# Kernel optimization log

Hardware: AMD Instinct MI355X
Metric: run time of the kernel (lower is better)

## Reference

```python
import jax, jax.numpy as jnp
import numpy as np

E = 16          # num_local_experts
K = 4           # experts_per_token
H = 2048        # hidden_size
I = 2048        # intermediate_size
LIMIT = 7.0     # swiglu_limit
ALPHA = 1.702   # glu_alpha


def setup_inputs() -> dict:
    key = jax.random.key(0)
    ks = jax.random.split(key, 9)
    int8 = lambda k, shp: jax.random.randint(k, shp, -127, 128).astype(jnp.float32)
    return {
        "hidden_states": jax.random.normal(ks[0], (1024, H), dtype=jnp.float32),
        "router_logits": jax.random.normal(ks[1], (1024, E), dtype=jnp.float32),
        "gate_up_proj": int8(ks[2], (E, H, 2 * I)),                      # int8 values in f32
        "gate_up_proj_scale": jax.random.uniform(ks[3], (E, 2 * I), minval=0.5, maxval=1.5) * 0.002,
        "gate_up_proj_bias": jax.random.normal(ks[4], (E, 2 * I), dtype=jnp.float32) * 0.01,
        "gate_up_smooth_scale": jnp.ones((E, I), dtype=jnp.float32),
        "down_proj": int8(ks[5], (E, I, H)),
        "down_proj_scale": jax.random.uniform(ks[6], (E, H), minval=0.5, maxval=1.5) * 0.002,
        "down_proj_bias": jax.random.normal(ks[7], (E, H), dtype=jnp.float32) * 0.01,
    }


def _dyn_quant(x):
    # per-token symmetric int8 dynamic quant (npu_dynamic_quant)
    scale = jnp.maximum(jnp.max(jnp.abs(x), axis=-1, keepdims=True) / 127.0, 1e-8)
    q = jnp.clip(jnp.round(x / scale), -127.0, 127.0)
    return q, scale


def reference(hidden_states, router_logits, gate_up_proj, gate_up_proj_scale,
              gate_up_proj_bias, gate_up_smooth_scale, down_proj,
              down_proj_scale, down_proj_bias):
    T = hidden_states.shape[0]
    C = (2 * T * K) // E

    # --- gating (npu_moe_gating_top_k: softmax + top-k, then renormalize) ---
    probs = jax.nn.softmax(router_logits, axis=-1)
    topk_w, topk_i = jax.lax.top_k(probs, K)                 # [T,K]
    topk_w = topk_w / jnp.sum(topk_w, axis=-1, keepdims=True)

    # --- per-token dynamic quant ---
    x_q, x_scale = _dyn_quant(hidden_states)                 # [T,H], [T,1]

    # --- dispatch (npu_moe_init_routing_v2): token-major expansion, capacity buckets ---
    flat_e = topk_i.reshape(-1)                              # [T*K] expert id per row
    flat_w = topk_w.reshape(-1)                              # [T*K]
    src = jnp.arange(T * K) // K                             # [T*K] source token
    onehot = jax.nn.one_hot(flat_e, E, dtype=jnp.int32)      # [T*K,E]
    pos = jnp.sum(jnp.cumsum(onehot, axis=0) * onehot, axis=1) - 1  # position within expert
    valid = pos < C
    slot = flat_e * C + jnp.where(valid, pos, 0)             # unique for valid rows
    vf = valid.astype(x_q.dtype)[:, None]
    x_disp = jnp.zeros((E * C, H), x_q.dtype).at[slot].add(x_q[src] * vf)
    s_disp = jnp.zeros((E * C, 1), x_scale.dtype).at[slot].add(x_scale[src] * vf)
    x_disp = x_disp.reshape(E, C, H)
    s_disp = s_disp.reshape(E, C, 1)

    gu_i32 = jnp.einsum('ech,ehf->ecf', x_disp, gate_up_proj)          # [E,C,2I]
    y = gu_i32 * s_disp * gate_up_proj_scale[:, None, :] + gate_up_proj_bias[:, None, :]

    # --- gpt-oss swiglu (activate_left, clamp_limit, alpha=1.702, glu_bias=1.0) ---
    gate = jnp.minimum(y[..., :I], LIMIT)
    up = jnp.clip(y[..., I:], -LIMIT, LIMIT)
    act = gate * jax.nn.sigmoid(ALPHA * gate) * (up + 1.0)
    act = act * gate_up_smooth_scale[:, None, :]

    # --- requant + grouped GEMM 2 + dequant ---
    h_q, h_scale = _dyn_quant(act)                                     # [E,C,I], [E,C,1]
    z_i32 = jnp.einsum('eci,eih->ech', h_q, down_proj)                 # [E,C,H]
    z = z_i32 * h_scale * down_proj_scale[:, None, :] + down_proj_bias[:, None, :]

    # --- combine (npu_moe_finalize_routing): weighted scatter-add per source token ---
    gathered = z.reshape(E * C, H)[slot]                               # [T*K,H]
    out = jnp.zeros((T, H), z.dtype).at[src].add(flat_w[:, None] * vf * gathered)
    return out
```

## Files before the change

### kernel.cpp

```cpp
#include <hip/hip_runtime.h>
#include <stdint.h>
#include <stddef.h>

#define T_TOK 1024
#define NE    16
#define TOPK  4
#define HID   2048
#define INTER 2048
#define CAP   512
#define GLIMIT 7.0f
#define GALPHA 1.702f

#define BM  128
#define BK  32
#define LDP 40

typedef __attribute__((ext_vector_type(8))) _Float16 half8;
typedef __attribute__((ext_vector_type(4))) float     f32x4;

__global__ __launch_bounds__(256) void gating_kernel(
    const float* __restrict__ logits, int* __restrict__ topki, float* __restrict__ topkw)
{
    int t = blockIdx.x * 256 + threadIdx.x;
    if (t >= T_TOK) return;
    float l[NE];
#pragma unroll
    for (int e = 0; e < NE; e++) l[e] = logits[t * NE + e];
    unsigned used = 0;
    float val[TOPK]; int idx[TOPK];
#pragma unroll
    for (int k = 0; k < TOPK; k++) {
        float bv = -3.4e38f; int bi = 0;
#pragma unroll
        for (int e = 0; e < NE; e++) {
            bool ok = (((used >> e) & 1u) == 0u) && (l[e] > bv);
            bv = ok ? l[e] : bv;
            bi = ok ? e : bi;
        }
        used |= (1u << bi); idx[k] = bi; val[k] = bv;
    }
    float m = val[0];
    float s = 0.f, w[TOPK];
#pragma unroll
    for (int k = 0; k < TOPK; k++) { w[k] = expf(val[k] - m); s += w[k]; }
    float inv = 1.0f / s;
#pragma unroll
    for (int k = 0; k < TOPK; k++) { topki[t * TOPK + k] = idx[k]; topkw[t * TOPK + k] = w[k] * inv; }
}

__global__ __launch_bounds__(256) void quant_x_kernel(
    const float* __restrict__ x, _Float16* __restrict__ xq, float* __restrict__ xs)
{
    int t = blockIdx.x;
    const float* row = x + (size_t)t * HID;
    __shared__ float red[256];
    float amax = 0.f;
    for (int i = threadIdx.x; i < HID; i += 256) amax = fmaxf(amax, fabsf(row[i]));
    red[threadIdx.x] = amax; __syncthreads();
    for (int s = 128; s > 0; s >>= 1) {
        if (threadIdx.x < s) red[threadIdx.x] = fmaxf(red[threadIdx.x], red[threadIdx.x + s]);
        __syncthreads();
    }
    float scale = fmaxf(red[0] / 127.0f, 1e-8f);
    if (threadIdx.x == 0) xs[t] = scale;
    for (int i = threadIdx.x; i < HID; i += 256) {
        float q = rintf(row[i] / scale);
        q = fminf(fmaxf(q, -127.f), 127.f);
        xq[(size_t)t * HID + i] = (_Float16)q;
    }
}

__global__ __launch_bounds__(1024) void routing_kernel(
    const int* __restrict__ topki, const float* __restrict__ topkw,
    int* __restrict__ row_src, float* __restrict__ row_w, int* __restrict__ counts)
{
    int wv = threadIdx.x >> 6;
    int lane = threadIdx.x & 63;
    int base = 0;
    for (int r0 = 0; r0 < T_TOK * TOPK; r0 += 64) {
        int r = r0 + lane;
        int e = topki[r];
        unsigned long long mask = __ballot(e == wv);
        int pre = __popcll(mask & ((1ULL << lane) - 1ULL));
        if (e == wv) {
            int pos = base + pre;
            if (pos < CAP) {
                row_src[wv * CAP + pos] = r >> 2;
                row_w[wv * CAP + pos] = topkw[r];
            }
        }
        base += __popcll(mask);
    }
    if (lane == 0) counts[wv] = (base < CAP) ? base : CAP;
}

__global__ __launch_bounds__(256) void gemm1_kernel(
    const _Float16* __restrict__ xq, const float* __restrict__ xs,
    const int* __restrict__ row_src, const int* __restrict__ counts,
    const float* __restrict__ gup, const float* __restrict__ gus,
    const float* __restrict__ gub, const float* __restrict__ smo,
    float* __restrict__ act)
{
    int nt = blockIdx.x;
    int mt = blockIdx.y;
    int e  = blockIdx.z;
    int count = counts[e];
    int m0 = mt * BM;
    if (m0 >= count) return;

    __shared__ _Float16 sA[BM * LDP];
    __shared__ _Float16 sB[128 * LDP];

    int t = threadIdx.x;
    int lane = t & 63, w = t >> 6;
    int n16 = lane & 15, quad = lane >> 4;

    int aM = t >> 1, aHalf = t & 1;
    int agr = m0 + aM;
    const _Float16* aptr = nullptr;
    if (agr < count) aptr = xq + (size_t)row_src[e * CAP + agr] * HID;

    f32x4 acc[2][8];
#pragma unroll
    for (int i = 0; i < 2; i++)
#pragma unroll
        for (int j = 0; j < 8; j++) acc[i][j] = (f32x4)0.0f;

    const float* gbase = gup + (size_t)e * HID * (2 * INTER);

    for (int k0 = 0; k0 < HID; k0 += BK) {
        __syncthreads();
        {
            int4 v0, v1;
            v0.x = v0.y = v0.z = v0.w = 0; v1 = v0;
            if (aptr) {
                const int4* s4 = (const int4*)(aptr + k0 + aHalf * 16);
                v0 = s4[0]; v1 = s4[1];
            }
            int4* d4 = (int4*)&sA[aM * LDP + aHalf * 16];
            d4[0] = v0; d4[1] = v1;
        }
        {
            int n = t & 63;
            int kr = (t >> 6) * 8;
#pragma unroll
            for (int h = 0; h < 2; h++) {
                const float* src = gbase + (size_t)(k0 + kr) * (2 * INTER) + h * INTER + nt * 64 + n;
#pragma unroll
                for (int i = 0; i < 8; i++)
                    sB[(h * 64 + n) * LDP + kr + i] = (_Float16)src[(size_t)i * (2 * INTER)];
            }
        }
        __syncthreads();

        half8 af[2], bfr[8];
#pragma unroll
        for (int mf = 0; mf < 2; mf++)
            af[mf] = *(const half8*)&sA[(w * 32 + mf * 16 + n16) * LDP + quad * 8];
#pragma unroll
        for (int nf = 0; nf < 8; nf++)
            bfr[nf] = *(const half8*)&sB[(nf * 16 + n16) * LDP + quad * 8];
#pragma unroll
        for (int mf = 0; mf < 2; mf++)
#pragma unroll
            for (int nf = 0; nf < 8; nf++)
                acc[mf][nf] = __builtin_amdgcn_mfma_f32_16x16x32_f16(af[mf], bfr[nf], acc[mf][nf], 0, 0, 0);
    }

    const float* gsc = gus + (size_t)e * (2 * INTER);
    const float* gbi = gub + (size_t)e * (2 * INTER);
    const float* sms = smo + (size_t)e * INTER;
#pragma unroll
    for (int mf = 0; mf < 2; mf++) {
#pragma unroll
        for (int r = 0; r < 4; r++) {
            int gr = m0 + w * 32 + mf * 16 + quad * 4 + r;
            if (gr >= count) continue;
            float srow = xs[row_src[e * CAP + gr]];
            float* arow = act + (size_t)(e * CAP + gr) * INTER;
#pragma unroll
            for (int g = 0; g < 4; g++) {
                int col = nt * 64 + g * 16 + n16;
                float yg = acc[mf][g][r]     * srow * gsc[col]         + gbi[col];
                float yu = acc[mf][g + 4][r] * srow * gsc[INTER + col] + gbi[INTER + col];
                float gate = fminf(yg, GLIMIT);
                float up   = fminf(fmaxf(yu, -GLIMIT), GLIMIT);
                float sig  = 1.0f / (1.0f + expf(-GALPHA * gate));
                arow[col] = gate * sig * (up + 1.0f) * sms[col];
            }
        }
    }
}

__global__ __launch_bounds__(256) void requant_kernel(
    const float* __restrict__ act, const int* __restrict__ counts,
    _Float16* __restrict__ hq, float* __restrict__ hs)
{
    int b = blockIdx.x;
    int e = b >> 9, c = b & (CAP - 1);
    if (c >= counts[e]) return;
    const float* row = act + (size_t)b * INTER;
    __shared__ float red[256];
    float amax = 0.f;
    for (int i = threadIdx.x; i < INTER; i += 256) amax = fmaxf(amax, fabsf(row[i]));
    red[threadIdx.x] = amax; __syncthreads();
    for (int s = 128; s > 0; s >>= 1) {
        if (threadIdx.x < s) red[threadIdx.x] = fmaxf(red[threadIdx.x], red[threadIdx.x + s]);
        __syncthreads();
    }
    float scale = fmaxf(red[0] / 127.0f, 1e-8f);
    if (threadIdx.x == 0) hs[b] = scale;
    for (int i = threadIdx.x; i < INTER; i += 256) {
        float q = rintf(row[i] / scale);
        q = fminf(fmaxf(q, -127.f), 127.f);
        hq[(size_t)b * INTER + i] = (_Float16)q;
    }
}

__global__ __launch_bounds__(256) void gemm2_kernel(
    const _Float16* __restrict__ hq, const float* __restrict__ hs,
    const int* __restrict__ row_src, const float* __restrict__ row_w,
    const int* __restrict__ counts, const float* __restrict__ dwn,
    const float* __restrict__ dsc, const float* __restrict__ dbi,
    float* __restrict__ out)
{
    int nt = blockIdx.x;
    int mt = blockIdx.y;
    int e  = blockIdx.z;
    int count = counts[e];
    int m0 = mt * BM;
    if (m0 >= count) return;

    __shared__ _Float16 sA[BM * LDP];
    __shared__ _Float16 sB[128 * LDP];

    int t = threadIdx.x;
    int lane = t & 63, w = t >> 6;
    int n16 = lane & 15, quad = lane >> 4;

    int aM = t >> 1, aHalf = t & 1;
    int agr = m0 + aM;
    const _Float16* aptr = nullptr;
    if (agr < count) aptr = hq + (size_t)(e * CAP + agr) * INTER;

    f32x4 acc[2][8];
#pragma unroll
    for (int i = 0; i < 2; i++)
#pragma unroll
        for (int j = 0; j < 8; j++) acc[i][j] = (f32x4)0.0f;

    const float* bbase = dwn + (size_t)e * INTER * HID;

    for (int k0 = 0; k0 < INTER; k0 += BK) {
        __syncthreads();
        {
            int4 v0, v1;
            v0.x = v0.y = v0.z = v0.w = 0; v1 = v0;
            if (aptr) {
                const int4* s4 = (const int4*)(aptr + k0 + aHalf * 16);
                v0 = s4[0]; v1 = s4[1];
            }
            int4* d4 = (int4*)&sA[aM * LDP + aHalf * 16];
            d4[0] = v0; d4[1] = v1;
        }
        {
            int n = t & 127;
            int kr = (t >> 7) * 16;
            const float* src = bbase + (size_t)(k0 + kr) * HID + nt * 128 + n;
#pragma unroll
            for (int i = 0; i < 16; i++)
                sB[n * LDP + kr + i] = (_Float16)src[(size_t)i * HID];
        }
        __syncthreads();

        half8 af[2], bfr[8];
#pragma unroll
        for (int mf = 0; mf < 2; mf++)
            af[mf] = *(const half8*)&sA[(w * 32 + mf * 16 + n16) * LDP + quad * 8];
#pragma unroll
        for (int nf = 0; nf < 8; nf++)
            bfr[nf] = *(const half8*)&sB[(nf * 16 + n16) * LDP + quad * 8];
#pragma unroll
        for (int mf = 0; mf < 2; mf++)
#pragma unroll
            for (int nf = 0; nf < 8; nf++)
                acc[mf][nf] = __builtin_amdgcn_mfma_f32_16x16x32_f16(af[mf], bfr[nf], acc[mf][nf], 0, 0, 0);
    }

    const float* dscE = dsc + (size_t)e * HID;
    const float* dbiE = dbi + (size_t)e * HID;
#pragma unroll
    for (int mf = 0; mf < 2; mf++) {
#pragma unroll
        for (int r = 0; r < 4; r++) {
            int gr = m0 + w * 32 + mf * 16 + quad * 4 + r;
            if (gr >= count) continue;
            int ri = e * CAP + gr;
            float hsr = hs[ri];
            float wr  = row_w[ri];
            float* orow = out + (size_t)row_src[ri] * HID;
#pragma unroll
            for (int nf = 0; nf < 8; nf++) {
                int col = nt * 128 + nf * 16 + n16;
                float z = acc[mf][nf][r] * hsr * dscE[col] + dbiE[col];
                atomicAdd(&orow[col], wr * z);
            }
        }
    }
}

extern "C" void kernel_launch(void* const* d_in, const int* in_sizes, int n_in,
                              void* d_out, int out_size, void* d_ws, size_t ws_size,
                              hipStream_t stream)
{
    (void)in_sizes; (void)n_in; (void)out_size; (void)ws_size;
    const float* x   = (const float*)d_in[0];
    const float* rl  = (const float*)d_in[1];
    const float* gup = (const float*)d_in[2];
    const float* gus = (const float*)d_in[3];
    const float* gub = (const float*)d_in[4];
    const float* smo = (const float*)d_in[5];
    const float* dwn = (const float*)d_in[6];
    const float* dsc = (const float*)d_in[7];
    const float* dbi = (const float*)d_in[8];
    float* out = (float*)d_out;

    char* p = (char*)d_ws;
    auto carve = [&](size_t bytes) -> char* {
        char* r = p; p += (bytes + 255) & ~(size_t)255; return r;
    };
    _Float16* xq   = (_Float16*)carve((size_t)T_TOK * HID * 2);
    float* xs      = (float*)carve((size_t)T_TOK * 4);
    int* topki     = (int*)carve((size_t)T_TOK * TOPK * 4);
    float* topkw   = (float*)carve((size_t)T_TOK * TOPK * 4);
    int* counts    = (int*)carve((size_t)NE * 4);
    int* rsrc      = (int*)carve((size_t)NE * CAP * 4);
    float* rw      = (float*)carve((size_t)NE * CAP * 4);
    float* actb    = (float*)carve((size_t)NE * CAP * INTER * 4);
    _Float16* hq   = (_Float16*)carve((size_t)NE * CAP * INTER * 2);
    float* hsb     = (float*)carve((size_t)NE * CAP * 4);

    hipMemsetAsync(d_out, 0, (size_t)T_TOK * HID * 4, stream);
    gating_kernel<<<dim3((T_TOK + 255) / 256), 256, 0, stream>>>(rl, topki, topkw);
    quant_x_kernel<<<dim3(T_TOK), 256, 0, stream>>>(x, xq, xs);
    routing_kernel<<<dim3(1), 1024, 0, stream>>>(topki, topkw, rsrc, rw, counts);
    gemm1_kernel<<<dim3(INTER / 64, CAP / BM, NE), 256, 0, stream>>>(
        xq, xs, rsrc, counts, gup, gus, gub, smo, actb);
    requant_kernel<<<dim3(NE * CAP), 256, 0, stream>>>(actb, counts, hq, hsb);
    gemm2_kernel<<<dim3(HID / 128, CAP / BM, NE), 256, 0, stream>>>(
        hq, hsb, rsrc, rw, counts, dwn, dsc, dbi, out);
}
```

Measured before the change: 1.081 ms.

## Switch grouped GEMMs to int8 MFMA with pre-packed int8 weight tiles

Result: no change. 1.094 ms (+1.2%).

```diff
diff --git a/kernel.cpp b/kernel.cpp
--- a/kernel.cpp
+++ b/kernel.cpp
@@ -12,11 +12,16 @@
 #define GALPHA 1.702f
 
 #define BM  128
-#define BK  32
-#define LDP 40
-
-typedef __attribute__((ext_vector_type(8))) _Float16 half8;
-typedef __attribute__((ext_vector_type(4))) float     f32x4;
+#define BK  64
+
+typedef __attribute__((ext_vector_type(4))) int   iv4;
+typedef __attribute__((ext_vector_type(4))) float f32x4;
+
+typedef const __attribute__((address_space(1))) unsigned gl_u32;
+typedef __attribute__((address_space(3))) unsigned lds_u32;
+__device__ __forceinline__ void gl_lds16(const void* g, void* l) {
+    __builtin_amdgcn_global_load_lds((gl_u32*)g, (lds_u32*)l, 16, 0, 0);
+}
 
 __global__ __launch_bounds__(256) void gating_kernel(
     const float* __restrict__ logits, int* __restrict__ topki, float* __restrict__ topkw)
@@ -49,13 +54,16 @@
 }
 
 __global__ __launch_bounds__(256) void quant_x_kernel(
-    const float* __restrict__ x, _Float16* __restrict__ xq, float* __restrict__ xs)
+    const float* __restrict__ x, char* __restrict__ xq, float* __restrict__ xs)
 {
     int t = blockIdx.x;
-    const float* row = x + (size_t)t * HID;
+    const float4* row = (const float4*)(x + (size_t)t * HID);
     __shared__ float red[256];
     float amax = 0.f;
-    for (int i = threadIdx.x; i < HID; i += 256) amax = fmaxf(amax, fabsf(row[i]));
+    float4 v0 = row[threadIdx.x];
+    float4 v1 = row[threadIdx.x + 256];
+    amax = fmaxf(amax, fmaxf(fmaxf(fabsf(v0.x), fabsf(v0.y)), fmaxf(fabsf(v0.z), fabsf(v0.w))));
+    amax = fmaxf(amax, fmaxf(fmaxf(fabsf(v1.x), fabsf(v1.y)), fmaxf(fabsf(v1.z), fabsf(v1.w))));
     red[threadIdx.x] = amax; __syncthreads();
     for (int s = 128; s > 0; s >>= 1) {
         if (threadIdx.x < s) red[threadIdx.x] = fmaxf(red[threadIdx.x], red[threadIdx.x + s]);
@@ -63,10 +71,19 @@
     }
     float scale = fmaxf(red[0] / 127.0f, 1e-8f);
     if (threadIdx.x == 0) xs[t] = scale;
-    for (int i = threadIdx.x; i < HID; i += 256) {
-        float q = rintf(row[i] / scale);
-        q = fminf(fmaxf(q, -127.f), 127.f);
-        xq[(size_t)t * HID + i] = (_Float16)q;
+    char4* orow = (char4*)(xq + (size_t)t * HID);
+    {
+        char4 c;
+        c.x = (char)fminf(fmaxf(rintf(v0.x / scale), -127.f), 127.f);
+        c.y = (char)fminf(fmaxf(rintf(v0.y / scale), -127.f), 127.f);
+        c.z = (char)fminf(fmaxf(rintf(v0.z / scale), -127.f), 127.f);
+        c.w = (char)fminf(fmaxf(rintf(v0.w / scale), -127.f), 127.f);
+        orow[threadIdx.x] = c;
+        c.x = (char)fminf(fmaxf(rintf(v1.x / scale), -127.f), 127.f);
+        c.y = (char)fminf(fmaxf(rintf(v1.y / scale), -127.f), 127.f);
+        c.z = (char)fminf(fmaxf(rintf(v1.z / scale), -127.f), 127.f);
+        c.w = (char)fminf(fmaxf(rintf(v1.w / scale), -127.f), 127.f);
+        orow[threadIdx.x + 256] = c;
     }
 }
 
@@ -94,10 +111,36 @@
     if (lane == 0) counts[wv] = (base < CAP) ? base : CAP;
 }
 
+__global__ __launch_bounds__(128) void convw_kernel(
+    const float* __restrict__ src, char* __restrict__ dst, int pitch, int mode)
+{
+    int nt = blockIdx.x, kt = blockIdx.y, e = blockIdx.z;
+    int l = threadIdx.x;
+    int col;
+    if (mode == 0) col = (l < 64) ? (nt * 64 + l) : (INTER + nt * 64 + (l - 64));
+    else           col = nt * 128 + l;
+    const float* s = src + (size_t)e * 2048 * pitch + (size_t)(kt * 64) * pitch + col;
+    int wv[16];
+#pragma unroll
+    for (int j = 0; j < 16; j++) {
+        int v = 0;
+#pragma unroll
+        for (int bq = 0; bq < 4; bq++) {
+            int q = (int)s[(size_t)(j * 4 + bq) * pitch];
+            v |= (q & 0xff) << (8 * bq);
+        }
+        wv[j] = v;
+    }
+    int4* d = (int4*)(dst + (((size_t)e * gridDim.x + nt) * 32 + kt) * 8192 + l * 64);
+#pragma unroll
+    for (int j = 0; j < 4; j++)
+        d[j] = make_int4(wv[4 * j], wv[4 * j + 1], wv[4 * j + 2], wv[4 * j + 3]);
+}
+
 __global__ __launch_bounds__(256) void gemm1_kernel(
-    const _Float16* __restrict__ xq, const float* __restrict__ xs,
+    const char* __restrict__ xq, const float* __restrict__ xs,
     const int* __restrict__ row_src, const int* __restrict__ counts,
-    const float* __restrict__ gup, const float* __restrict__ gus,
+    const char* __restrict__ gpack, const float* __restrict__ gus,
     const float* __restrict__ gub, const float* __restrict__ smo,
     float* __restrict__ act)
 {
@@ -108,63 +151,52 @@
     int m0 = mt * BM;
     if (m0 >= count) return;
 
-    __shared__ _Float16 sA[BM * LDP];
-    __shared__ _Float16 sB[128 * LDP];
+    __shared__ char sA[BM * BK];
+    __shared__ char sB[128 * BK];
 
     int t = threadIdx.x;
     int lane = t & 63, w = t >> 6;
     int n16 = lane & 15, quad = lane >> 4;
 
-    int aM = t >> 1, aHalf = t & 1;
-    int agr = m0 + aM;
-    const _Float16* aptr = nullptr;
-    if (agr < count) aptr = xq + (size_t)row_src[e * CAP + agr] * HID;
-
-    f32x4 acc[2][8];
+    const char* aSrc[2];
+#pragma unroll
+    for (int op = 0; op < 2; op++) {
+        int c = op * 256 + t;
+        int row = c >> 2, ks = c & 3;
+        int gr = m0 + row;
+        if (gr > count - 1) gr = count - 1;
+        aSrc[op] = xq + (size_t)row_src[e * CAP + gr] * HID + ks * 16;
+    }
+    const char* bSrc = gpack + (((size_t)e * 32 + nt) * 32) * 8192 + t * 16;
+
+    iv4 acc[2][8];
 #pragma unroll
     for (int i = 0; i < 2; i++)
 #pragma unroll
-        for (int j = 0; j < 8; j++) acc[i][j] = (f32x4)0.0f;
-
-    const float* gbase = gup + (size_t)e * HID * (2 * INTER);
-
-    for (int k0 = 0; k0 < HID; k0 += BK) {
-        __syncthreads();
-        {
-            int4 v0, v1;
-            v0.x = v0.y = v0.z = v0.w = 0; v1 = v0;
-            if (aptr) {
-                const int4* s4 = (const int4*)(aptr + k0 + aHalf * 16);
-                v0 = s4[0]; v1 = s4[1];
-            }
-            int4* d4 = (int4*)&sA[aM * LDP + aHalf * 16];
-            d4[0] = v0; d4[1] = v1;
-        }
-        {
-            int n = t & 63;
-            int kr = (t >> 6) * 8;
-#pragma unroll
-            for (int h = 0; h < 2; h++) {
-                const float* src = gbase + (size_t)(k0 + kr) * (2 * INTER) + h * INTER + nt * 64 + n;
-#pragma unroll
-                for (int i = 0; i < 8; i++)
-                    sB[(h * 64 + n) * LDP + kr + i] = (_Float16)src[(size_t)i * (2 * INTER)];
-            }
-        }
-        __syncthreads();
-
-        half8 af[2], bfr[8];
+        for (int j = 0; j < 8; j++) acc[i][j] = (iv4)0;
+
+    for (int kt = 0; kt < HID / BK; kt++) {
+        __syncthreads();
+#pragma unroll
+        for (int op = 0; op < 2; op++)
+            gl_lds16(aSrc[op] + kt * BK, sA + op * 4096 + w * 1024);
+#pragma unroll
+        for (int op = 0; op < 2; op++)
+            gl_lds16(bSrc + kt * 8192 + op * 4096, sB + op * 4096 + w * 1024);
+        __syncthreads();
+
+        iv4 af[2], bf[8];
 #pragma unroll
         for (int mf = 0; mf < 2; mf++)
-            af[mf] = *(const half8*)&sA[(w * 32 + mf * 16 + n16) * LDP + quad * 8];
+            af[mf] = *(const iv4*)(sA + (w * 32 + mf * 16 + n16) * 64 + quad * 16);
 #pragma unroll
         for (int nf = 0; nf < 8; nf++)
-            bfr[nf] = *(const half8*)&sB[(nf * 16 + n16) * LDP + quad * 8];
+            bf[nf] = *(const iv4*)(sB + (nf * 16 + n16) * 64 + quad * 16);
 #pragma unroll
         for (int mf = 0; mf < 2; mf++)
 #pragma unroll
             for (int nf = 0; nf < 8; nf++)
-                acc[mf][nf] = __builtin_amdgcn_mfma_f32_16x16x32_f16(af[mf], bfr[nf], acc[mf][nf], 0, 0, 0);
+                acc[mf][nf] = __builtin_amdgcn_mfma_i32_16x16x64_i8(af[mf], bf[nf], acc[mf][nf], 0, 0, 0);
     }
 
     const float* gsc = gus + (size_t)e * (2 * INTER);
@@ -181,8 +213,8 @@
 #pragma unroll
             for (int g = 0; g < 4; g++) {
                 int col = nt * 64 + g * 16 + n16;
-                float yg = acc[mf][g][r]     * srow * gsc[col]         + gbi[col];
-                float yu = acc[mf][g + 4][r] * srow * gsc[INTER + col] + gbi[INTER + col];
+                float yg = (float)acc[mf][g][r]     * srow * gsc[col]         + gbi[col];
+                float yu = (float)acc[mf][g + 4][r] * srow * gsc[INTER + col] + gbi[INTER + col];
                 float gate = fminf(yg, GLIMIT);
                 float up   = fminf(fmaxf(yu, -GLIMIT), GLIMIT);
                 float sig  = 1.0f / (1.0f + expf(-GALPHA * gate));
@@ -194,15 +226,17 @@
 
 __global__ __launch_bounds__(256) void requant_kernel(
     const float* __restrict__ act, const int* __restrict__ counts,
-    _Float16* __restrict__ hq, float* __restrict__ hs)
+    char* __restrict__ hq, float* __restrict__ hs)
 {
     int b = blockIdx.x;
     int e = b >> 9, c = b & (CAP - 1);
     if (c >= counts[e]) return;
-    const float* row = act + (size_t)b * INTER;
+    const float4* row = (const float4*)(act + (size_t)b * INTER);
     __shared__ float red[256];
-    float amax = 0.f;
-    for (int i = threadIdx.x; i < INTER; i += 256) amax = fmaxf(amax, fabsf(row[i]));
+    float4 v0 = row[threadIdx.x];
+    float4 v1 = row[threadIdx.x + 256];
+    float amax = fmaxf(fmaxf(fabsf(v0.x), fabsf(v0.y)), fmaxf(fabsf(v0.z), fabsf(v0.w)));
+    amax = fmaxf(amax, fmaxf(fmaxf(fabsf(v1.x), fabsf(v1.y)), fmaxf(fabsf(v1.z), fabsf(v1.w))));
     red[threadIdx.x] = amax; __syncthreads();
     for (int s = 128; s > 0; s >>= 1) {
         if (threadIdx.x < s) red[threadIdx.x] = fmaxf(red[threadIdx.x], red[threadIdx.x + s]);
@@ -210,17 +244,26 @@
     }
     float scale = fmaxf(red[0] / 127.0f, 1e-8f);
     if (threadIdx.x == 0) hs[b] = scale;
-    for (int i = threadIdx.x; i < INTER; i += 256) {
-        float q = rintf(row[i] / scale);
-        q = fminf(fmaxf(q, -127.f), 127.f);
-        hq[(size_t)b * INTER + i] = (_Float16)q;
+    char4* orow = (char4*)(hq + (size_t)b * INTER);
+    {
+        char4 cc;
+        cc.x = (char)fminf(fmaxf(rintf(v0.x / scale), -127.f), 127.f);
+        cc.y = (char)fminf(fmaxf(rintf(v0.y / scale), -127.f), 127.f);
+        cc.z = (char)fminf(fmaxf(rintf(v0.z / scale), -127.f), 127.f);
+        cc.w = (char)fminf(fmaxf(rintf(v0.w / scale), -127.f), 127.f);
+        orow[threadIdx.x] = cc;
+        cc.x = (char)fminf(fmaxf(rintf(v1.x / scale), -127.f), 127.f);
+        cc.y = (char)fminf(fmaxf(rintf(v1.y / scale), -127.f), 127.f);
+        cc.z = (char)fminf(fmaxf(rintf(v1.z / scale), -127.f), 127.f);
+        cc.w = (char)fminf(fmaxf(rintf(v1.w / scale), -127.f), 127.f);
+        orow[threadIdx.x + 256] = cc;
     }
 }
 
 __global__ __launch_bounds__(256) void gemm2_kernel(
-    const _Float16* __restrict__ hq, const float* __restrict__ hs,
+    const char* __restrict__ hq, const float* __restrict__ hs,
     const int* __restrict__ row_src, const float* __restrict__ row_w,
-    const int* __restrict__ counts, const float* __restrict__ dwn,
+    const int* __restrict__ counts, const char* __restrict__ dpack,
     const float* __restrict__ dsc, const float* __restrict__ dbi,
     float* __restrict__ out)
 {
@@ -231,60 +274,52 @@
     int m0 = mt * BM;
     if (m0 >= count) return;
 
-    __shared__ _Float16 sA[BM * LDP];
-    __shared__ _Float16 sB[128 * LDP];
+    __shared__ char sA[BM * BK];
+    __shared__ char sB[128 * BK];
 
     int t = threadIdx.x;
     int lane = t & 63, w = t >> 6;
     int n16 = lane & 15, quad = lane >> 4;
 
-    int aM = t >> 1, aHalf = t & 1;
-    int agr = m0 + aM;
-    const _Float16* aptr = nullptr;
-    if (agr < count) aptr = hq + (size_t)(e * CAP + agr) * INTER;
-
-    f32x4 acc[2][8];
+    const char* aSrc[2];
+#pragma unroll
+    for (int op = 0; op < 2; op++) {
+        int c = op * 256 + t;
+        int row = c >> 2, ks = c & 3;
+        int gr = m0 + row;
+        if (gr > count - 1) gr = count - 1;
+        aSrc[op] = hq + (size_t)(e * CAP + gr) * INTER + ks * 16;
+    }
+    const char* bSrc = dpack + (((size_t)e * 16 + nt) * 32) * 8192 + t * 16;
+
+    iv4 acc[2][8];
 #pragma unroll
     for (int i = 0; i < 2; i++)
 #pragma unroll
-        for (int j = 0; j < 8; j++) acc[i][j] = (f32x4)0.0f;
-
-    const float* bbase = dwn + (size_t)e * INTER * HID;
-
-    for (int k0 = 0; k0 < INTER; k0 += BK) {
-        __syncthreads();
-        {
-            int4 v0, v1;
-            v0.x = v0.y = v0.z = v0.w = 0; v1 = v0;
-            if (aptr) {
-                const int4* s4 = (const int4*)(aptr + k0 + aHalf * 16);
-                v0 = s4[0]; v1 = s4[1];
-            }
-            int4* d4 = (int4*)&sA[aM * LDP + aHalf * 16];
-            d4[0] = v0; d4[1] = v1;
-        }
-        {
-            int n = t & 127;
-            int kr = (t >> 7) * 16;
-            const float* src = bbase + (size_t)(k0 + kr) * HID + nt * 128 + n;
-#pragma unroll
-            for (int i = 0; i < 16; i++)
-                sB[n * LDP + kr + i] = (_Float16)src[(size_t)i * HID];
-        }
-        __syncthreads();
-
-        half8 af[2], bfr[8];
+        for (int j = 0; j < 8; j++) acc[i][j] = (iv4)0;
+
+    for (int kt = 0; kt < INTER / BK; kt++) {
+        __syncthreads();
+#pragma unroll
+        for (int op = 0; op < 2; op++)
+            gl_lds16(aSrc[op] + kt * BK, sA + op * 4096 + w * 1024);
+#pragma unroll
+        for (int op = 0; op < 2; op++)
+            gl_lds16(bSrc + kt * 8192 + op * 4096, sB + op * 4096 + w * 1024);
+        __syncthreads();
+
+        iv4 af[2], bf[8];
 #pragma unroll
         for (int mf = 0; mf < 2; mf++)
-            af[mf] = *(const half8*)&sA[(w * 32 + mf * 16 + n16) * LDP + quad * 8];
+            af[mf] = *(const iv4*)(sA + (w * 32 + mf * 16 + n16) * 64 + quad * 16);
 #pragma unroll
         for (int nf = 0; nf < 8; nf++)
-            bfr[nf] = *(const half8*)&sB[(nf * 16 + n16) * LDP + quad * 8];
+            bf[nf] = *(const iv4*)(sB + (nf * 16 + n16) * 64 + quad * 16);
 #pragma unroll
         for (int mf = 0; mf < 2; mf++)
 #pragma unroll
             for (int nf = 0; nf < 8; nf++)
-                acc[mf][nf] = __builtin_amdgcn_mfma_f32_16x16x32_f16(af[mf], bfr[nf], acc[mf][nf], 0, 0, 0);
+                acc[mf][nf] = __builtin_amdgcn_mfma_i32_16x16x64_i8(af[mf], bf[nf], acc[mf][nf], 0, 0, 0);
     }
 
     const float* dscE = dsc + (size_t)e * HID;
@@ -302,7 +337,7 @@
 #pragma unroll
             for (int nf = 0; nf < 8; nf++) {
                 int col = nt * 128 + nf * 16 + n16;
-                float z = acc[mf][nf][r] * hsr * dscE[col] + dbiE[col];
+                float z = (float)acc[mf][nf][r] * hsr * dscE[col] + dbiE[col];
                 atomicAdd(&orow[col], wr * z);
             }
         }
@@ -329,7 +364,7 @@
     auto carve = [&](size_t bytes) -> char* {
         char* r = p; p += (bytes + 255) & ~(size_t)255; return r;
     };
-    _Float16* xq   = (_Float16*)carve((size_t)T_TOK * HID * 2);
+    char* xq       = carve((size_t)T_TOK * HID);
     float* xs      = (float*)carve((size_t)T_TOK * 4);
     int* topki     = (int*)carve((size_t)T_TOK * TOPK * 4);
     float* topkw   = (float*)carve((size_t)T_TOK * TOPK * 4);
@@ -337,16 +372,20 @@
     int* rsrc      = (int*)carve((size_t)NE * CAP * 4);
     float* rw      = (float*)carve((size_t)NE * CAP * 4);
     float* actb    = (float*)carve((size_t)NE * CAP * INTER * 4);
-    _Float16* hq   = (_Float16*)carve((size_t)NE * CAP * INTER * 2);
+    char* hq       = carve((size_t)NE * CAP * INTER);
     float* hsb     = (float*)carve((size_t)NE * CAP * 4);
+    char* gpack    = carve((size_t)NE * 32 * 32 * 8192);
+    char* dpack    = carve((size_t)NE * 16 * 32 * 8192);
 
     hipMemsetAsync(d_out, 0, (size_t)T_TOK * HID * 4, stream);
     gating_kernel<<<dim3((T_TOK + 255) / 256), 256, 0, stream>>>(rl, topki, topkw);
     quant_x_kernel<<<dim3(T_TOK), 256, 0, stream>>>(x, xq, xs);
     routing_kernel<<<dim3(1), 1024, 0, stream>>>(topki, topkw, rsrc, rw, counts);
+    convw_kernel<<<dim3(32, 32, NE), 128, 0, stream>>>(gup, gpack, 2 * INTER, 0);
+    convw_kernel<<<dim3(16, 32, NE), 128, 0, stream>>>(dwn, dpack, HID, 1);
     gemm1_kernel<<<dim3(INTER / 64, CAP / BM, NE), 256, 0, stream>>>(
-        xq, xs, rsrc, counts, gup, gus, gub, smo, actb);
+        xq, xs, rsrc, counts, gpack, gus, gub, smo, actb);
     requant_kernel<<<dim3(NE * CAP), 256, 0, stream>>>(actb, counts, hq, hsb);
     gemm2_kernel<<<dim3(HID / 128, CAP / BM, NE), 256, 0, stream>>>(
-        hq, hsb, rsrc, rw, counts, dwn, dsc, dbi, out);
-}
+        hq, hsb, rsrc, rw, counts, dpack, dsc, dbi, out);
+}
```
